# Kernel optimization log

Hardware: AMD Instinct MI355X
Metric: run time of the kernel (lower is better)

The kernel has to match this reference:

```python
import jax, jax.numpy as jnp
import numpy as np

STAGES = 3
CAUSAL = True


def sine_positional_encoding(T, D, dtype=jnp.float32):
    # keras_nlp SinePositionEncoding: interleaved sin/cos, base 10000
    pos = jnp.arange(T, dtype=dtype)[:, None]            # [T,1]
    i = jnp.arange(D)[None, :]                            # [1,D]
    angle = pos / jnp.power(jnp.asarray(10000.0, dtype), (2 * (i // 2)).astype(dtype) / D)
    return jnp.where(i % 2 == 0, jnp.sin(angle), jnp.cos(angle))  # [T,D]


def setup_inputs() -> dict:
    key = jax.random.key(0)
    kX, kWp, kbp, kWf, kbf = jax.random.split(key, 5)
    B, T, D = 4, 4096, 1024
    X = jax.random.normal(kX, (B, T, D), dtype=jnp.float32)
    # data_projection: D -> (stages+1)*D
    Wp = jax.random.normal(kWp, (D, (STAGES + 1) * D), dtype=jnp.float32) / np.sqrt(D)
    bp = jnp.zeros(((STAGES + 1) * D,), dtype=jnp.float32)
    # filters: D -> stages*D (applied to positional encoding)
    Wf = jax.random.normal(kWf, (D, STAGES * D), dtype=jnp.float32) / np.sqrt(D)
    bf = jnp.zeros((STAGES * D,), dtype=jnp.float32)
    return {"X": X, "Wp": Wp, "bp": bp, "Wf": Wf, "bf": bf}


def reference(X, Wp, bp, Wf, bf):
    B, T, D = X.shape
    # linear projections of data: [B,T,stages+1,D]
    xp = (jnp.einsum('btd,de->bte', X, Wp) + bp).reshape(B, T, STAGES + 1, D)
    # filters from sinusoidal positional encoding (batch-independent): [T,stages,D]
    pos = sine_positional_encoding(T, D, X.dtype)
    f = (pos @ Wf + bf).reshape(T, STAGES, D)
    if CAUSAL:
        # zero-pad time axis to 2T -> circular FFT conv becomes linear (causal) conv
        xp = jnp.concatenate([xp, jnp.zeros_like(xp)], axis=1)   # [B,2T,S+1,D]
        f = jnp.concatenate([f, jnp.zeros_like(f)], axis=0)      # [2T,S,D]
    L = xp.shape[1]
    F = jnp.fft.rfft(f, axis=0)                                   # [L//2+1,S,D]
    y = xp[:, :, 0, :]                                            # [B,L,D]
    for i in range(STAGES):
        conv = jnp.fft.irfft(jnp.fft.rfft(y, axis=1) * F[None, :, i, :], n=L, axis=1)
        y = conv * xp[:, :, i + 1, :]
    return y[:, :T, :] if CAUSAL else y
```

## Files before the change

kernel.cpp:

```cpp
#include <hip/hip_runtime.h>
#include <math.h>

#define T_LEN 4096
#define D_DIM 1024
#define B_DIM 4
#define N_STAGES 3
#define FT 512

typedef unsigned short bf16_t;
typedef __bf16 bf16x8 __attribute__((ext_vector_type(8)));
typedef float f32x4 __attribute__((ext_vector_type(4)));

#define SW(i) ((i) ^ ((((unsigned)(i)) >> 4) & 15))

__device__ __forceinline__ bf16_t f2bf(float f) {
    union { float f; unsigned u; } v; v.f = f;
    unsigned r = v.u + 0x7FFFu + ((v.u >> 16) & 1u);
    return (bf16_t)(r >> 16);
}
__device__ __forceinline__ float bf2f(bf16_t h) {
    union { unsigned u; float f; } v; v.u = ((unsigned)h) << 16;
    return v.f;
}
__device__ __forceinline__ float2 cmul(float2 a, float2 b) {
    return make_float2(a.x * b.x - a.y * b.y, a.x * b.y + a.y * b.x);
}
__device__ __forceinline__ float2 cadd(float2 a, float2 b) { return make_float2(a.x + b.x, a.y + b.y); }
__device__ __forceinline__ float2 csub(float2 a, float2 b) { return make_float2(a.x - b.x, a.y - b.y); }
__device__ __forceinline__ float2 conjf2(float2 a) { return make_float2(a.x, -a.y); }

#define GLOAD_LDS16(gp, lp) __builtin_amdgcn_global_load_lds( \
    (const __attribute__((address_space(1))) void*)(gp),      \
    (__attribute__((address_space(3))) void*)(lp), 16, 0, 0)

__global__ __launch_bounds__(256) void pos_kernel(bf16_t* __restrict__ posbf) {
    int idx = blockIdx.x * 256 + threadIdx.x;
    int t = idx >> 10;
    int k = idx & 1023;
    float e = (float)(k & ~1) / (float)D_DIM;
    float r = exp2f(-e * 13.287712379549449f);
    float angle = (float)t * r;
    float v = (k & 1) ? cosf(angle) : sinf(angle);
    posbf[idx] = f2bf(v);
}

__global__ __launch_bounds__(256) void f32_to_bf16_kernel(const float* __restrict__ in,
                                                          bf16_t* __restrict__ out, int n8) {
    int i = blockIdx.x * 256 + threadIdx.x;
    if (i >= n8) return;
    float4 a = ((const float4*)in)[i * 2];
    float4 b = ((const float4*)in)[i * 2 + 1];
    ((ushort4*)out)[i * 2]     = make_ushort4(f2bf(a.x), f2bf(a.y), f2bf(a.z), f2bf(a.w));
    ((ushort4*)out)[i * 2 + 1] = make_ushort4(f2bf(b.x), f2bf(b.y), f2bf(b.z), f2bf(b.w));
}

__global__ __launch_bounds__(256) void transpose_to_bf16(const float* __restrict__ in,
                                                         bf16_t* __restrict__ out, int K, int N) {
    __shared__ float tile[32][33];
    const int n0 = blockIdx.x * 32;
    const int k0 = blockIdx.y * 32;
    const int tx = threadIdx.x & 31;
    const int ty = threadIdx.x >> 5;
    for (int i = ty; i < 32; i += 8)
        tile[i][tx] = in[(size_t)(k0 + i) * N + n0 + tx];
    __syncthreads();
    for (int i = ty; i < 32; i += 8)
        out[(size_t)(n0 + i) * K + k0 + tx] = f2bf(tile[tx][i]);
}

template <int MODE>
__global__ __launch_bounds__(256) void mfma_gemm(const bf16_t* __restrict__ A,
                                                 const bf16_t* __restrict__ BT,
                                                 const float* __restrict__ bias,
                                                 void* __restrict__ outv,
                                                 int M, int N, int K, int nbx) {
    constexpr int SMEM_BYTES = (MODE == 0) ? (128 * 136 * 2) : (128 * 132 * 4);
    __shared__ __align__(16) char smem[SMEM_BYTES];
    bf16_t* As = (bf16_t*)smem;
    bf16_t* Bs = (bf16_t*)(smem + 8192);

    const int tid = threadIdx.x;
    const int lane = tid & 63;
    const int w = tid >> 6;
    const int wr = w >> 1, wc = w & 1;

    const int nwg = gridDim.x;
    const int q = nwg >> 3;
    const int swz = (blockIdx.x & 7) * q + (blockIdx.x >> 3);
    const int by = swz / nbx, bx = swz - by * nbx;
    const int row0 = by * 128, col0 = bx * 128;

    f32x4 acc[4][4];
#pragma unroll
    for (int m = 0; m < 4; ++m)
#pragma unroll
        for (int n = 0; n < 4; ++n) acc[m][n] = (f32x4)(0.0f);

    int offs[2], rr[2], kk8[2];
#pragma unroll
    for (int c = 0; c < 2; ++c) {
        offs[c] = (w * 2 + c) * 1024 + lane * 16;
        rr[c] = offs[c] >> 6;
        kk8[c] = ((offs[c] >> 4) & 3) * 8;
    }

    for (int k0 = 0; k0 < K; k0 += 32) {
#pragma unroll
        for (int c = 0; c < 2; ++c) {
            const bf16_t* gA = A + (size_t)(row0 + rr[c]) * K + k0 + kk8[c];
            GLOAD_LDS16(gA, As + (w * 2 + c) * 512);
            const bf16_t* gB = BT + (size_t)(col0 + rr[c]) * K + k0 + kk8[c];
            GLOAD_LDS16(gB, Bs + (w * 2 + c) * 512);
        }
        __syncthreads();

        bf16x8 af[4], bfr[4];
#pragma unroll
        for (int m = 0; m < 4; ++m)
            af[m] = *(const bf16x8*)&As[(wr * 64 + m * 16 + (lane & 15)) * 32 + (lane >> 4) * 8];
#pragma unroll
        for (int n = 0; n < 4; ++n)
            bfr[n] = *(const bf16x8*)&Bs[(wc * 64 + n * 16 + (lane & 15)) * 32 + (lane >> 4) * 8];
#pragma unroll
        for (int m = 0; m < 4; ++m)
#pragma unroll
            for (int n = 0; n < 4; ++n)
                acc[m][n] = __builtin_amdgcn_mfma_f32_16x16x32_bf16(af[m], bfr[n], acc[m][n], 0, 0, 0);
        __syncthreads();
    }

    if (MODE == 0) {
        bf16_t* Cs = (bf16_t*)smem;
#pragma unroll
        for (int m = 0; m < 4; ++m)
#pragma unroll
            for (int n = 0; n < 4; ++n) {
                int cl = wc * 64 + n * 16 + (lane & 15);
                int rlb = wr * 64 + m * 16 + ((lane >> 4) << 2);
                float bb = bias[col0 + cl];
#pragma unroll
                for (int j = 0; j < 4; ++j)
                    Cs[cl * 136 + rlb + j] = f2bf(acc[m][n][j] + bb);
            }
        __syncthreads();
        int dl = tid >> 1, th = tid & 1;
        int cc = col0 + dl;
        int s = cc >> 10, d = cc & 1023;
        int b = row0 >> 12;
        int t0 = (row0 & 4095) + th * 64;
        uint4* dst = (uint4*)&((bf16_t*)outv)[((size_t)(s * 4 + b) * 1024 + d) * 4096 + t0];
        const uint4* src = (const uint4*)&Cs[dl * 136 + th * 64];
#pragma unroll
        for (int j = 0; j < 8; ++j) dst[j] = src[j];
    } else {
        float* CsF = (float*)smem;
#pragma unroll
        for (int m = 0; m < 4; ++m)
#pragma unroll
            for (int n = 0; n < 4; ++n) {
                int cl = wc * 64 + n * 16 + (lane & 15);
                int rlb = wr * 64 + m * 16 + ((lane >> 4) << 2);
                float bb = bias[col0 + cl];
#pragma unroll
                for (int j = 0; j < 4; ++j)
                    CsF[cl * 132 + rlb + j] = acc[m][n][j] + bb;
            }
        __syncthreads();
        int dl = tid >> 1, th = tid & 1;
        int cc = col0 + dl;
        uint4* dst = (uint4*)&((float*)outv)[(size_t)cc * 4096 + row0 + th * 64];
        const uint4* src = (const uint4*)&CsF[dl * 132 + th * 64];
#pragma unroll
        for (int j = 0; j < 16; ++j) dst[j] = src[j];
    }
}

template <int INV>
__device__ __forceinline__ void bfly4(float2& a, float2& b, float2& c, float2& d) {
    float2 t0 = cadd(a, c), t1 = csub(a, c), t2 = cadd(b, d), t3 = csub(b, d);
    float2 it3 = INV ? make_float2(-t3.y, t3.x) : make_float2(t3.y, -t3.x);
    a = cadd(t0, t2); b = cadd(t1, it3); c = csub(t0, t2); d = csub(t1, it3);
}

template <int INV, int M>
__device__ __forceinline__ void r8_pass(float2* __restrict__ s, const float2* __restrict__ Wq) {
    const int p = threadIdx.x;
    const int r = p & (M - 1);
    const int jm = p - r;
    float2 x0 = s[SW(p)];
    float2 x1 = s[SW(p + 512)];
    float2 x2 = s[SW(p + 1024)];
    float2 x3 = s[SW(p + 1536)];
    float2 x4 = s[SW(p + 2048)];
    float2 x5 = s[SW(p + 2560)];
    float2 x6 = s[SW(p + 3072)];
    float2 x7 = s[SW(p + 3584)];
    __syncthreads();

    bfly4<INV>(x0, x2, x4, x6);
    bfly4<INV>(x1, x3, x5, x7);
    const float s2 = 0.70710678118654752f;
    const float2 o1 = INV ? make_float2(s2, s2) : make_float2(s2, -s2);
    const float2 o3 = INV ? make_float2(-s2, s2) : make_float2(-s2, -s2);
    x3 = cmul(x3, o1);
    x5 = INV ? make_float2(-x5.y, x5.x) : make_float2(x5.y, -x5.x);
    x7 = cmul(x7, o3);
    float2 F0 = cadd(x0, x1), F4 = csub(x0, x1);
    float2 F1 = cadd(x2, x3), F5 = csub(x2, x3);
    float2 F2 = cadd(x4, x5), F6 = csub(x4, x5);
    float2 F3 = cadd(x6, x7), F7 = csub(x6, x7);

    const int base = 8 * jm + r;
    if (M == 512) {
        s[SW(base)]           = F0;
        s[SW(base + 512)]     = F1;
        s[SW(base + 2 * 512)] = F2;
        s[SW(base + 3 * 512)] = F3;
        s[SW(base + 4 * 512)] = F4;
        s[SW(base + 5 * 512)] = F5;
        s[SW(base + 6 * 512)] = F6;
        s[SW(base + 7 * 512)] = F7;
    } else {
        float2 w1 = Wq[jm];
        if (INV) w1.y = -w1.y;
        s[SW(base)]         = F0;
        s[SW(base + M)]     = cmul(w1, F1);
        float2 w2 = cmul(w1, w1);
        s[SW(base + 2 * M)] = cmul(w2, F2);
        float2 w3 = cmul(w2, w1);
        s[SW(base + 3 * M)] = cmul(w3, F3);
        float2 w4 = cmul(w2, w2);
        s[SW(base + 4 * M)] = cmul(w4, F4);
        s[SW(base + 5 * M)] = cmul(cmul(w4, w1), F5);
        float2 w6 = cmul(w4, w2);
        s[SW(base + 6 * M)] = cmul(w6, F6);
        s[SW(base + 7 * M)] = cmul(cmul(w6, w1), F7);
    }
    __syncthreads();
}

template <int INV>
__device__ __forceinline__ void fft4096_ip(float2* __restrict__ s, const float2* __restrict__ Wq) {
    r8_pass<INV, 1>(s, Wq);
    r8_pass<INV, 8>(s, Wq);
    r8_pass<INV, 64>(s, Wq);
    r8_pass<INV, 512>(s, Wq);
}

__device__ __forceinline__ void init_tables(float2* __restrict__ Wq, float2* __restrict__ Wu) {
    const int tid = threadIdx.x;
    {
        float sn, cs;
        __sincosf((float)tid * -1.5339807878856412e-3f, &sn, &cs);
        Wq[tid] = make_float2(cs, sn);
    }
#pragma unroll
    for (int u = 0; u < 4; ++u) {
        int k = u * FT + tid;
        float sn, cs;
        __sincosf((float)k * -7.669903939428206e-4f, &sn, &cs);
        Wu[k] = make_float2(cs, sn);
    }
}

__device__ __forceinline__ float2 spec_load(const void* spec, int bf, size_t row, int k) {
    if (bf) {
        ushort2 h = ((const ushort2*)spec)[row * 4097 + k];
        return make_float2(bf2f(h.x), bf2f(h.y));
    }
    return ((const float2*)spec)[row * 4097 + k];
}
__device__ __forceinline__ void spec_store(void* spec, int bf, size_t row, int k, float2 v) {
    if (bf) ((ushort2*)spec)[row * 4097 + k] = make_ushort2(f2bf(v.x), f2bf(v.y));
    else    ((float2*)spec)[row * 4097 + k] = v;
}

__global__ __launch_bounds__(FT)
void filter_fft_kernel(const float* __restrict__ fT,
                       void* __restrict__ specv,
                       int spec_bf16) {
    __shared__ __align__(16) float2 sA[4096];
    __shared__ float2 Wq[512];
    __shared__ float2 Wu[2048];
    const int tid = threadIdx.x;
    const size_t row = blockIdx.x;
    init_tables(Wq, Wu);
    const float4* f4 = (const float4*)&fT[row * T_LEN];
#pragma unroll
    for (int u = 0; u < 2; ++u) {
        int j = u * FT + tid;
        float4 v = f4[j];
        sA[SW(2 * j)]     = make_float2(v.x, v.y);
        sA[SW(2 * j + 1)] = make_float2(v.z, v.w);
    }
#pragma unroll
    for (int u = 0; u < 4; ++u) {
        int n = 2048 + u * FT + tid;
        sA[SW(n)] = make_float2(0.0f, 0.0f);
    }
    __syncthreads();
    fft4096_ip<0>(sA, Wq);
#pragma unroll
    for (int u = 0; u < 4; ++u) {
        int s = u * FT + tid;
        if (s < 2047) {
            int k = s + 1, nk = 4096 - k;
            float2 Zk = sA[SW(k)], Zn = sA[SW(nk)];
            float2 Ye = make_float2(0.5f * (Zk.x + Zn.x), 0.5f * (Zk.y - Zn.y));
            float2 Yo = make_float2(0.5f * (Zk.y + Zn.y), -0.5f * (Zk.x - Zn.x));
            float2 w = Wu[k];
            float2 wYo = cmul(w, Yo);
            spec_store(specv, spec_bf16, row, k, cadd(Ye, wYo));
            spec_store(specv, spec_bf16, row, nk, conjf2(csub(Ye, wYo)));
        }
    }
    if (tid == 0) {
        float2 Z0 = sA[SW(0)];
        spec_store(specv, spec_bf16, row, 0,    make_float2(Z0.x + Z0.y, 0.0f));
        spec_store(specv, spec_bf16, row, 4096, make_float2(Z0.x - Z0.y, 0.0f));
        spec_store(specv, spec_bf16, row, 2048, conjf2(sA[SW(2048)]));
    }
}

__global__ __launch_bounds__(FT)
void conv_kernel(const bf16_t* __restrict__ xpT,
                 const void* __restrict__ specv,
                 int spec_bf16,
                 bf16_t* __restrict__ yT) {
    __shared__ __align__(16) float2 sA[4096];
    __shared__ float2 Wq[512];
    __shared__ float2 Wu[2048];
    const int tid = threadIdx.x;
    const int bid = blockIdx.x;
    const int b = bid >> 10;
    const int d = bid & 1023;
    init_tables(Wq, Wu);

    const ushort4* y4 = (const ushort4*)&xpT[((size_t)b * 1024 + d) * T_LEN];
#pragma unroll
    for (int u = 0; u < 2; ++u) {
        int j = u * FT + tid;
        ushort4 h = y4[j];
        sA[SW(2 * j)]     = make_float2(bf2f(h.x), bf2f(h.y));
        sA[SW(2 * j + 1)] = make_float2(bf2f(h.z), bf2f(h.w));
    }
#pragma unroll
    for (int u = 0; u < 4; ++u) {
        int n = 2048 + u * FT + tid;
        sA[SW(n)] = make_float2(0.0f, 0.0f);
    }
    __syncthreads();

    const float scale = 1.0f / 4096.0f;
    for (int st = 0; st < N_STAGES; ++st) {
        fft4096_ip<0>(sA, Wq);
        const size_t row = (size_t)st * 1024 + d;
#pragma unroll
        for (int u = 0; u < 4; ++u) {
            int s = u * FT + tid;
            if (s < 2047) {
                int k = s + 1, nk = 4096 - k;
                float2 Zk = sA[SW(k)], Zn = sA[SW(nk)];
                float2 Ye = make_float2(0.5f * (Zk.x + Zn.x), 0.5f * (Zk.y - Zn.y));
                float2 Yo = make_float2(0.5f * (Zk.y + Zn.y), -0.5f * (Zk.x - Zn.x));
                float2 w = Wu[k];
                float2 wYo = cmul(w, Yo);
                float2 Yk = cadd(Ye, wYo);
                float2 Ynk = conjf2(csub(Ye, wYo));
                float2 Fk = spec_load(specv, spec_bf16, row, k);
                float2 Fn = spec_load(specv, spec_bf16, row, nk);
                float2 Hk = cmul(Yk, Fk);
                float2 Hn = cmul(Ynk, Fn);
                float2 He = make_float2(0.5f * (Hk.x + Hn.x), 0.5f * (Hk.y - Hn.y));
                float2 Hd = make_float2(0.5f * (Hk.x - Hn.x), 0.5f * (Hk.y + Hn.y));
                float2 Ho = cmul(conjf2(w), Hd);
                sA[SW(k)]  = make_float2(He.x - Ho.y, He.y + Ho.x);
                sA[SW(nk)] = make_float2(He.x + Ho.y, Ho.x - He.y);
            }
        }
        if (tid == 0) {
            float2 Z0 = sA[SW(0)];
            float Y0 = Z0.x + Z0.y, YN = Z0.x - Z0.y;
            float2 F0 = spec_load(specv, spec_bf16, row, 0);
            float2 FN = spec_load(specv, spec_bf16, row, 4096);
            float2 H0 = make_float2(Y0 * F0.x, Y0 * F0.y);
            float2 HN = make_float2(YN * FN.x, YN * FN.y);
            float2 He0 = make_float2(0.5f * (H0.x + HN.x), 0.5f * (H0.y + HN.y));
            float2 Ho0 = make_float2(0.5f * (H0.x - HN.x), 0.5f * (H0.y - HN.y));
            sA[SW(0)] = make_float2(He0.x - Ho0.y, He0.y + Ho0.x);
            float2 H2 = cmul(conjf2(sA[SW(2048)]), spec_load(specv, spec_bf16, row, 2048));
            sA[SW(2048)] = conjf2(H2);
        }
        __syncthreads();
        fft4096_ip<1>(sA, Wq);

        const ushort4* g4 = (const ushort4*)&xpT[((size_t)((st + 1) * 4 + b) * 1024 + d) * T_LEN];
        if (st < N_STAGES - 1) {
#pragma unroll
            for (int u = 0; u < 2; ++u) {
                int j = u * FT + tid;
                ushort4 h = g4[j];
                float2 v0 = sA[SW(2 * j)], v1 = sA[SW(2 * j + 1)];
                sA[SW(2 * j)]     = make_float2(v0.x * scale * bf2f(h.x), v0.y * scale * bf2f(h.y));
                sA[SW(2 * j + 1)] = make_float2(v1.x * scale * bf2f(h.z), v1.y * scale * bf2f(h.w));
            }
#pragma unroll
            for (int u = 0; u < 4; ++u) {
                int n = 2048 + u * FT + tid;
                sA[SW(n)] = make_float2(0.0f, 0.0f);
            }
            __syncthreads();
        } else {
            ushort4* yrow = (ushort4*)&yT[((size_t)b * 1024 + d) * T_LEN];
#pragma unroll
            for (int u = 0; u < 2; ++u) {
                int j = u * FT + tid;
                ushort4 h = g4[j];
                float2 v0 = sA[SW(2 * j)], v1 = sA[SW(2 * j + 1)];
                yrow[j] = make_ushort4(f2bf(v0.x * scale * bf2f(h.x)),
                                       f2bf(v0.y * scale * bf2f(h.y)),
                                       f2bf(v1.x * scale * bf2f(h.z)),
                                       f2bf(v1.y * scale * bf2f(h.w)));
            }
        }
    }
}

__global__ __launch_bounds__(256) void transpose_out(const bf16_t* __restrict__ yT,
                                                     float* __restrict__ out) {
    __shared__ float tile[32][33];
    const int tb = blockIdx.z;
    const int t0 = blockIdx.x * 32;
    const int d0 = blockIdx.y * 32;
    const int tx = threadIdx.x & 31;
    const int ty = threadIdx.x >> 5;
    for (int i = ty; i < 32; i += 8)
        tile[i][tx] = bf2f(yT[((size_t)tb * 1024 + d0 + i) * 4096 + t0 + tx]);
    __syncthreads();
    for (int i = ty; i < 32; i += 8)
        out[((size_t)tb * 4096 + t0 + i) * 1024 + d0 + tx] = tile[tx][i];
}

extern "C" void kernel_launch(void* const* d_in, const int* in_sizes, int n_in,
                              void* d_out, int out_size, void* d_ws, size_t ws_size,
                              hipStream_t stream) {
    const float* X   = (const float*)d_in[0];
    const float* Wp  = (const float*)d_in[1];
    const float* bp  = (const float*)d_in[2];
    const float* Wf  = (const float*)d_in[3];
    const float* bfv = (const float*)d_in[4];
    float* out = (float*)d_out;
    char* ws = (char*)d_ws;

    const size_t XPT_BYTES  = (size_t)134217728;
    const size_t SPEC_F32_B = (size_t)3 * 1024 * 4097 * 8;
    const size_t SPEC_BF_B  = (size_t)3 * 1024 * 4097 * 4;
    const size_t XBF_BYTES  = (size_t)33554432;
    const size_t WPT_BYTES  = (size_t)8388608;

    bf16_t* xpT   = (bf16_t*)ws;
    bf16_t* posbf = (bf16_t*)ws;
    bf16_t* WfT   = (bf16_t*)(ws + 16777216);
    float*  fT    = (float*)(ws + 33554432);
    void*   spec  = (void*)(ws + XPT_BYTES);

    int spec_bf16;
    size_t spec_bytes;
    if (ws_size >= XPT_BYTES + SPEC_F32_B + XBF_BYTES + WPT_BYTES) {
        spec_bf16 = 0; spec_bytes = SPEC_F32_B;
    } else {
        spec_bf16 = 1; spec_bytes = SPEC_BF_B;
    }
    bf16_t* Xbf = (bf16_t*)(ws + XPT_BYTES + spec_bytes);
    bf16_t* WpT = (bf16_t*)(ws + XPT_BYTES + spec_bytes + XBF_BYTES);
    bf16_t* yT  = Xbf;

    pos_kernel<<<(T_LEN * D_DIM) / 256, 256, 0, stream>>>(posbf);

    transpose_to_bf16<<<dim3(3072 / 32, 1024 / 32), 256, 0, stream>>>(Wf, WfT, 1024, 3072);
    mfma_gemm<1><<<768, 256, 0, stream>>>(posbf, WfT, bfv, fT, 4096, 3072, 1024, 24);

    filter_fft_kernel<<<N_STAGES * D_DIM, FT, 0, stream>>>(fT, spec, spec_bf16);

    f32_to_bf16_kernel<<<8192, 256, 0, stream>>>(X, Xbf, 2097152);
    transpose_to_bf16<<<dim3(4096 / 32, 1024 / 32), 256, 0, stream>>>(Wp, WpT, 1024, 4096);
    mfma_gemm<0><<<4096, 256, 0, stream>>>(Xbf, WpT, bp, xpT, 16384, 4096, 1024, 32);

    conv_kernel<<<B_DIM * D_DIM, FT, 0, stream>>>(xpT, spec, spec_bf16, yT);

    transpose_out<<<dim3(4096 / 32, 1024 / 32, B_DIM), 256, 0, stream>>>(yT, out);
}
```

Baseline: 805.7 us.

## Batch all four sequences per conv block to share filter spectrum loads

The conv kernel now gives each block one channel d and processes all four batch rows in four shared-memory FFT buffers. Each radix-8 pass loads and transforms the four sequences together, so twiddles, the filter spectrum loads and the table setup are amortised across the batch. The grid shrinks from B*D to D blocks. The cost is a shared-memory footprint of about 148KB per block, which allows far fewer resident blocks per CU, plus higher register pressure from holding 32 complex values per thread.

```diff
diff --git a/kernel.cpp b/kernel.cpp
--- a/kernel.cpp
+++ b/kernel.cpp
@@ -182,59 +182,52 @@
     a = cadd(t0, t2); b = cadd(t1, it3); c = csub(t0, t2); d = csub(t1, it3);
 }
 
+template <int INV>
+__device__ __forceinline__ void dft8(float2 (&x)[8]) {
+    bfly4<INV>(x[0], x[2], x[4], x[6]);
+    bfly4<INV>(x[1], x[3], x[5], x[7]);
+    const float s2 = 0.70710678118654752f;
+    const float2 o1 = INV ? make_float2(s2, s2) : make_float2(s2, -s2);
+    const float2 o3 = INV ? make_float2(-s2, s2) : make_float2(-s2, -s2);
+    x[3] = cmul(x[3], o1);
+    x[5] = INV ? make_float2(-x[5].y, x[5].x) : make_float2(x[5].y, -x[5].x);
+    x[7] = cmul(x[7], o3);
+    float2 F0 = cadd(x[0], x[1]), F4 = csub(x[0], x[1]);
+    float2 F1 = cadd(x[2], x[3]), F5 = csub(x[2], x[3]);
+    float2 F2 = cadd(x[4], x[5]), F6 = csub(x[4], x[5]);
+    float2 F3 = cadd(x[6], x[7]), F7 = csub(x[6], x[7]);
+    x[0] = F0; x[1] = F1; x[2] = F2; x[3] = F3;
+    x[4] = F4; x[5] = F5; x[6] = F6; x[7] = F7;
+}
+
 template <int INV, int M>
 __device__ __forceinline__ void r8_pass(float2* __restrict__ s, const float2* __restrict__ Wq) {
     const int p = threadIdx.x;
     const int r = p & (M - 1);
     const int jm = p - r;
-    float2 x0 = s[SW(p)];
-    float2 x1 = s[SW(p + 512)];
-    float2 x2 = s[SW(p + 1024)];
-    float2 x3 = s[SW(p + 1536)];
-    float2 x4 = s[SW(p + 2048)];
-    float2 x5 = s[SW(p + 2560)];
-    float2 x6 = s[SW(p + 3072)];
-    float2 x7 = s[SW(p + 3584)];
-    __syncthreads();
-
-    bfly4<INV>(x0, x2, x4, x6);
-    bfly4<INV>(x1, x3, x5, x7);
-    const float s2 = 0.70710678118654752f;
-    const float2 o1 = INV ? make_float2(s2, s2) : make_float2(s2, -s2);
-    const float2 o3 = INV ? make_float2(-s2, s2) : make_float2(-s2, -s2);
-    x3 = cmul(x3, o1);
-    x5 = INV ? make_float2(-x5.y, x5.x) : make_float2(x5.y, -x5.x);
-    x7 = cmul(x7, o3);
-    float2 F0 = cadd(x0, x1), F4 = csub(x0, x1);
-    float2 F1 = cadd(x2, x3), F5 = csub(x2, x3);
-    float2 F2 = cadd(x4, x5), F6 = csub(x4, x5);
-    float2 F3 = cadd(x6, x7), F7 = csub(x6, x7);
-
+    float2 x[8];
+#pragma unroll
+    for (int c = 0; c < 8; ++c) x[c] = s[SW(p + 512 * c)];
+    __syncthreads();
+    dft8<INV>(x);
     const int base = 8 * jm + r;
     if (M == 512) {
-        s[SW(base)]           = F0;
-        s[SW(base + 512)]     = F1;
-        s[SW(base + 2 * 512)] = F2;
-        s[SW(base + 3 * 512)] = F3;
-        s[SW(base + 4 * 512)] = F4;
-        s[SW(base + 5 * 512)] = F5;
-        s[SW(base + 6 * 512)] = F6;
-        s[SW(base + 7 * 512)] = F7;
+#pragma unroll
+        for (int q = 0; q < 8; ++q) s[SW(base + q * 512)] = x[q];
     } else {
         float2 w1 = Wq[jm];
         if (INV) w1.y = -w1.y;
-        s[SW(base)]         = F0;
-        s[SW(base + M)]     = cmul(w1, F1);
         float2 w2 = cmul(w1, w1);
-        s[SW(base + 2 * M)] = cmul(w2, F2);
         float2 w3 = cmul(w2, w1);
-        s[SW(base + 3 * M)] = cmul(w3, F3);
         float2 w4 = cmul(w2, w2);
-        s[SW(base + 4 * M)] = cmul(w4, F4);
-        s[SW(base + 5 * M)] = cmul(cmul(w4, w1), F5);
-        float2 w6 = cmul(w4, w2);
-        s[SW(base + 6 * M)] = cmul(w6, F6);
-        s[SW(base + 7 * M)] = cmul(cmul(w6, w1), F7);
+        s[SW(base)]         = x[0];
+        s[SW(base + M)]     = cmul(w1, x[1]);
+        s[SW(base + 2 * M)] = cmul(w2, x[2]);
+        s[SW(base + 3 * M)] = cmul(w3, x[3]);
+        s[SW(base + 4 * M)] = cmul(w4, x[4]);
+        s[SW(base + 5 * M)] = cmul(cmul(w4, w1), x[5]);
+        s[SW(base + 6 * M)] = cmul(cmul(w4, w2), x[6]);
+        s[SW(base + 7 * M)] = cmul(cmul(w4, w3), x[7]);
     }
     __syncthreads();
 }
@@ -245,6 +238,60 @@
     r8_pass<INV, 8>(s, Wq);
     r8_pass<INV, 64>(s, Wq);
     r8_pass<INV, 512>(s, Wq);
+}
+
+template <int INV, int M>
+__device__ __forceinline__ void r8_pass4(float2 (*__restrict__ s)[4096],
+                                         const float2* __restrict__ Wq) {
+    const int p = threadIdx.x;
+    const int r = p & (M - 1);
+    const int jm = p - r;
+    float2 x[4][8];
+#pragma unroll
+    for (int bb = 0; bb < 4; ++bb)
+#pragma unroll
+        for (int c = 0; c < 8; ++c) x[bb][c] = s[bb][SW(p + 512 * c)];
+    __syncthreads();
+    const int base = 8 * jm + r;
+    if (M == 512) {
+#pragma unroll
+        for (int bb = 0; bb < 4; ++bb) {
+            dft8<INV>(x[bb]);
+#pragma unroll
+            for (int q = 0; q < 8; ++q) s[bb][SW(base + q * 512)] = x[bb][q];
+        }
+    } else {
+        float2 w1 = Wq[jm];
+        if (INV) w1.y = -w1.y;
+        float2 w2 = cmul(w1, w1);
+        float2 w3 = cmul(w2, w1);
+        float2 w4 = cmul(w2, w2);
+        float2 w5 = cmul(w4, w1);
+        float2 w6 = cmul(w4, w2);
+        float2 w7 = cmul(w4, w3);
+#pragma unroll
+        for (int bb = 0; bb < 4; ++bb) {
+            dft8<INV>(x[bb]);
+            s[bb][SW(base)]         = x[bb][0];
+            s[bb][SW(base + M)]     = cmul(w1, x[bb][1]);
+            s[bb][SW(base + 2 * M)] = cmul(w2, x[bb][2]);
+            s[bb][SW(base + 3 * M)] = cmul(w3, x[bb][3]);
+            s[bb][SW(base + 4 * M)] = cmul(w4, x[bb][4]);
+            s[bb][SW(base + 5 * M)] = cmul(w5, x[bb][5]);
+            s[bb][SW(base + 6 * M)] = cmul(w6, x[bb][6]);
+            s[bb][SW(base + 7 * M)] = cmul(w7, x[bb][7]);
+        }
+    }
+    __syncthreads();
+}
+
+template <int INV>
+__device__ __forceinline__ void fft4096_ip4(float2 (*__restrict__ s)[4096],
+                                            const float2* __restrict__ Wq) {
+    r8_pass4<INV, 1>(s, Wq);
+    r8_pass4<INV, 8>(s, Wq);
+    r8_pass4<INV, 64>(s, Wq);
+    r8_pass4<INV, 512>(s, Wq);
 }
 
 __device__ __forceinline__ void init_tables(float2* __restrict__ Wq, float2* __restrict__ Wu) {
@@ -327,100 +374,116 @@
                  const void* __restrict__ specv,
                  int spec_bf16,
                  bf16_t* __restrict__ yT) {
-    __shared__ __align__(16) float2 sA[4096];
+    __shared__ __align__(16) float2 sA[4][4096];
     __shared__ float2 Wq[512];
     __shared__ float2 Wu[2048];
     const int tid = threadIdx.x;
-    const int bid = blockIdx.x;
-    const int b = bid >> 10;
-    const int d = bid & 1023;
+    const int d = blockIdx.x;
     init_tables(Wq, Wu);
 
-    const ushort4* y4 = (const ushort4*)&xpT[((size_t)b * 1024 + d) * T_LEN];
-#pragma unroll
-    for (int u = 0; u < 2; ++u) {
-        int j = u * FT + tid;
-        ushort4 h = y4[j];
-        sA[SW(2 * j)]     = make_float2(bf2f(h.x), bf2f(h.y));
-        sA[SW(2 * j + 1)] = make_float2(bf2f(h.z), bf2f(h.w));
-    }
-#pragma unroll
-    for (int u = 0; u < 4; ++u) {
-        int n = 2048 + u * FT + tid;
-        sA[SW(n)] = make_float2(0.0f, 0.0f);
+#pragma unroll
+    for (int bb = 0; bb < 4; ++bb) {
+        const ushort4* y4 = (const ushort4*)&xpT[((size_t)bb * 1024 + d) * T_LEN];
+#pragma unroll
+        for (int u = 0; u < 2; ++u) {
+            int j = u * FT + tid;
+            ushort4 h = y4[j];
+            sA[bb][SW(2 * j)]     = make_float2(bf2f(h.x), bf2f(h.y));
+            sA[bb][SW(2 * j + 1)] = make_float2(bf2f(h.z), bf2f(h.w));
+        }
+#pragma unroll
+        for (int u = 0; u < 4; ++u) {
+            int n = 2048 + u * FT + tid;
+            sA[bb][SW(n)] = make_float2(0.0f, 0.0f);
+        }
     }
     __syncthreads();
 
     const float scale = 1.0f / 4096.0f;
     for (int st = 0; st < N_STAGES; ++st) {
-        fft4096_ip<0>(sA, Wq);
+        fft4096_ip4<0>(sA, Wq);
         const size_t row = (size_t)st * 1024 + d;
 #pragma unroll
         for (int u = 0; u < 4; ++u) {
             int s = u * FT + tid;
             if (s < 2047) {
                 int k = s + 1, nk = 4096 - k;
-                float2 Zk = sA[SW(k)], Zn = sA[SW(nk)];
-                float2 Ye = make_float2(0.5f * (Zk.x + Zn.x), 0.5f * (Zk.y - Zn.y));
-                float2 Yo = make_float2(0.5f * (Zk.y + Zn.y), -0.5f * (Zk.x - Zn.x));
                 float2 w = Wu[k];
-                float2 wYo = cmul(w, Yo);
-                float2 Yk = cadd(Ye, wYo);
-                float2 Ynk = conjf2(csub(Ye, wYo));
+                float2 cw = conjf2(w);
                 float2 Fk = spec_load(specv, spec_bf16, row, k);
                 float2 Fn = spec_load(specv, spec_bf16, row, nk);
-                float2 Hk = cmul(Yk, Fk);
-                float2 Hn = cmul(Ynk, Fn);
-                float2 He = make_float2(0.5f * (Hk.x + Hn.x), 0.5f * (Hk.y - Hn.y));
-                float2 Hd = make_float2(0.5f * (Hk.x - Hn.x), 0.5f * (Hk.y + Hn.y));
-                float2 Ho = cmul(conjf2(w), Hd);
-                sA[SW(k)]  = make_float2(He.x - Ho.y, He.y + Ho.x);
-                sA[SW(nk)] = make_float2(He.x + Ho.y, Ho.x - He.y);
+#pragma unroll
+                for (int bb = 0; bb < 4; ++bb) {
+                    float2 Zk = sA[bb][SW(k)], Zn = sA[bb][SW(nk)];
+                    float2 Ye = make_float2(0.5f * (Zk.x + Zn.x), 0.5f * (Zk.y - Zn.y));
+                    float2 Yo = make_float2(0.5f * (Zk.y + Zn.y), -0.5f * (Zk.x - Zn.x));
+                    float2 wYo = cmul(w, Yo);
+                    float2 Yk = cadd(Ye, wYo);
+                    float2 Ynk = conjf2(csub(Ye, wYo));
+                    float2 Hk = cmul(Yk, Fk);
+                    float2 Hn = cmul(Ynk, Fn);
+                    float2 He = make_float2(0.5f * (Hk.x + Hn.x), 0.5f * (Hk.y - Hn.y));
+                    float2 Hd = make_float2(0.5f * (Hk.x - Hn.x), 0.5f * (Hk.y + Hn.y));
+                    float2 Ho = cmul(cw, Hd);
+                    sA[bb][SW(k)]  = make_float2(He.x - Ho.y, He.y + Ho.x);
+                    sA[bb][SW(nk)] = make_float2(He.x + Ho.y, Ho.x - He.y);
+                }
             }
         }
         if (tid == 0) {
-            float2 Z0 = sA[SW(0)];
-            float Y0 = Z0.x + Z0.y, YN = Z0.x - Z0.y;
             float2 F0 = spec_load(specv, spec_bf16, row, 0);
             float2 FN = spec_load(specv, spec_bf16, row, 4096);
-            float2 H0 = make_float2(Y0 * F0.x, Y0 * F0.y);
-            float2 HN = make_float2(YN * FN.x, YN * FN.y);
-            float2 He0 = make_float2(0.5f * (H0.x + HN.x), 0.5f * (H0.y + HN.y));
-            float2 Ho0 = make_float2(0.5f * (H0.x - HN.x), 0.5f * (H0.y - HN.y));
-            sA[SW(0)] = make_float2(He0.x - Ho0.y, He0.y + Ho0.x);
-            float2 H2 = cmul(conjf2(sA[SW(2048)]), spec_load(specv, spec_bf16, row, 2048));
-            sA[SW(2048)] = conjf2(H2);
+            float2 F2 = spec_load(specv, spec_bf16, row, 2048);
+#pragma unroll
+            for (int bb = 0; bb < 4; ++bb) {
+                float2 Z0 = sA[bb][SW(0)];
+                float Y0 = Z0.x + Z0.y, YN = Z0.x - Z0.y;
+                float2 H0 = make_float2(Y0 * F0.x, Y0 * F0.y);
+                float2 HN = make_float2(YN * FN.x, YN * FN.y);
+                float2 He0 = make_float2(0.5f * (H0.x + HN.x), 0.5f * (H0.y + HN.y));
+                float2 Ho0 = make_float2(0.5f * (H0.x - HN.x), 0.5f * (H0.y - HN.y));
+                sA[bb][SW(0)] = make_float2(He0.x - Ho0.y, He0.y + Ho0.x);
+                float2 H2 = cmul(conjf2(sA[bb][SW(2048)]), F2);
+                sA[bb][SW(2048)] = conjf2(H2);
+            }
         }
         __syncthreads();
-        fft4096_ip<1>(sA, Wq);
-
-        const ushort4* g4 = (const ushort4*)&xpT[((size_t)((st + 1) * 4 + b) * 1024 + d) * T_LEN];
+        fft4096_ip4<1>(sA, Wq);
+
         if (st < N_STAGES - 1) {
 #pragma unroll
-            for (int u = 0; u < 2; ++u) {
-                int j = u * FT + tid;
-                ushort4 h = g4[j];
-                float2 v0 = sA[SW(2 * j)], v1 = sA[SW(2 * j + 1)];
-                sA[SW(2 * j)]     = make_float2(v0.x * scale * bf2f(h.x), v0.y * scale * bf2f(h.y));
-                sA[SW(2 * j + 1)] = make_float2(v1.x * scale * bf2f(h.z), v1.y * scale * bf2f(h.w));
-            }
-#pragma unroll
-            for (int u = 0; u < 4; ++u) {
-                int n = 2048 + u * FT + tid;
-                sA[SW(n)] = make_float2(0.0f, 0.0f);
+            for (int bb = 0; bb < 4; ++bb) {
+                const ushort4* g4 = (const ushort4*)&xpT[((size_t)((st + 1) * 4 + bb) * 1024 + d) * T_LEN];
+#pragma unroll
+                for (int u = 0; u < 2; ++u) {
+                    int j = u * FT + tid;
+                    ushort4 h = g4[j];
+                    float2 v0 = sA[bb][SW(2 * j)], v1 = sA[bb][SW(2 * j + 1)];
+                    sA[bb][SW(2 * j)]     = make_float2(v0.x * scale * bf2f(h.x), v0.y * scale * bf2f(h.y));
+                    sA[bb][SW(2 * j + 1)] = make_float2(v1.x * scale * bf2f(h.z), v1.y * scale * bf2f(h.w));
+                }
+#pragma unroll
+                for (int u = 0; u < 4; ++u) {
+                    int n = 2048 + u * FT + tid;
+                    sA[bb][SW(n)] = make_float2(0.0f, 0.0f);
+                }
             }
             __syncthreads();
         } else {
-            ushort4* yrow = (ushort4*)&yT[((size_t)b * 1024 + d) * T_LEN];
-#pragma unroll
-            for (int u = 0; u < 2; ++u) {
-                int j = u * FT + tid;
-                ushort4 h = g4[j];
-                float2 v0 = sA[SW(2 * j)], v1 = sA[SW(2 * j + 1)];
-                yrow[j] = make_ushort4(f2bf(v0.x * scale * bf2f(h.x)),
-                                       f2bf(v0.y * scale * bf2f(h.y)),
-                                       f2bf(v1.x * scale * bf2f(h.z)),
-                                       f2bf(v1.y * scale * bf2f(h.w)));
+#pragma unroll
+            for (int bb = 0; bb < 4; ++bb) {
+                const ushort4* g4 = (const ushort4*)&xpT[((size_t)((st + 1) * 4 + bb) * 1024 + d) * T_LEN];
+                ushort4* yrow = (ushort4*)&yT[((size_t)bb * 1024 + d) * T_LEN];
+#pragma unroll
+                for (int u = 0; u < 2; ++u) {
+                    int j = u * FT + tid;
+                    ushort4 h = g4[j];
+                    float2 v0 = sA[bb][SW(2 * j)], v1 = sA[bb][SW(2 * j + 1)];
+                    yrow[j] = make_ushort4(f2bf(v0.x * scale * bf2f(h.x)),
+                                           f2bf(v0.y * scale * bf2f(h.y)),
+                                           f2bf(v1.x * scale * bf2f(h.z)),
+                                           f2bf(v1.y * scale * bf2f(h.w)));
+                }
             }
         }
     }
@@ -486,7 +549,7 @@
     transpose_to_bf16<<<dim3(4096 / 32, 1024 / 32), 256, 0, stream>>>(Wp, WpT, 1024, 4096);
     mfma_gemm<0><<<4096, 256, 0, stream>>>(Xbf, WpT, bp, xpT, 16384, 4096, 1024, 32);
 
-    conv_kernel<<<B_DIM * D_DIM, FT, 0, stream>>>(xpT, spec, spec_bf16, yT);
+    conv_kernel<<<D_DIM, FT, 0, stream>>>(xpT, spec, spec_bf16, yT);
 
     transpose_out<<<dim3(4096 / 32, 1024 / 32, B_DIM), 256, 0, stream>>>(yT, out);
 }
```

Measured after the change: 683.2 us. 1.18x faster.
